# Performance work log

Measured on AMD Instinct MI355X. Metric: run time of the kernel, lower is better.

The kernel has to match this reference:

```python
import jax, jax.numpy as jnp
import numpy as np

N, L, E, H = 2, 2048, 1024, 16
DH = E // H  # head_dim = 64


def setup_inputs() -> dict:
    key = jax.random.key(0)
    ks = jax.random.split(key, 11)
    s_h = 1.0 / np.sqrt(DH)
    s_e = 1.0 / np.sqrt(E)
    return {
        "EP_q": jax.random.normal(ks[0], (N, L, E), jnp.float32),
        "EP_k": jax.random.normal(ks[1], (N, L, E), jnp.float32),
        "EP_v": jax.random.normal(ks[2], (N, L, E), jnp.float32),
        "W_q": jax.random.uniform(ks[3], (DH, DH), jnp.float32, -s_h, s_h),
        "b_q": jax.random.uniform(ks[4], (DH,), jnp.float32, -s_h, s_h),
        "W_k": jax.random.uniform(ks[5], (DH, DH), jnp.float32, -s_h, s_h),
        "b_k": jax.random.uniform(ks[6], (DH,), jnp.float32, -s_h, s_h),
        "W_v": jax.random.uniform(ks[7], (DH, DH), jnp.float32, -s_h, s_h),
        "b_v": jax.random.uniform(ks[8], (DH,), jnp.float32, -s_h, s_h),
        "W_o": jax.random.uniform(ks[9], (E, E), jnp.float32, -s_e, s_e),
        "b_o": jax.random.uniform(ks[10], (E,), jnp.float32, -s_e, s_e),
    }


def reference(EP_q, EP_k, EP_v, W_q, b_q, W_k, b_k, W_v, b_v, W_o, b_o):
    n, q_len = EP_q.shape[0], EP_q.shape[1]
    # split into heads: (N, L, H, DH)
    q = EP_q.reshape(n, q_len, H, DH)
    k = EP_k.reshape(n, EP_k.shape[1], H, DH)
    v = EP_v.reshape(n, EP_v.shape[1], H, DH)
    # per-head linear (same weights across heads), torch Linear: x @ W.T + b
    Q = q @ W_q.T + b_q
    K = k @ W_k.T + b_k
    V = v @ W_v.T + b_v
    # scores (N, H, Lq, Lk); NOTE: scaled by sqrt(embed_size) per original code
    scores = jnp.einsum("nqhd,nkhd->nhqk", Q, K) / jnp.sqrt(jnp.float32(E))
    attn = jax.nn.softmax(scores, axis=-1)
    out = jnp.einsum("nhqk,nkhd->nqhd", attn, V).reshape(n, q_len, E)
    return out @ W_o.T + b_o
```

## Files before the change

### kernel.cpp

```cpp
#include <hip/hip_runtime.h>

#define N_B 2
#define L_L 2048
#define E_E 1024
#define H_H 16
#define D_H 64
#define LDSP 72

typedef __bf16 bf16x8 __attribute__((ext_vector_type(8)));
typedef float f32x4 __attribute__((ext_vector_type(4)));
typedef short s16x8 __attribute__((ext_vector_type(8)));
typedef unsigned short u16x4 __attribute__((ext_vector_type(4)));

__device__ __forceinline__ f32x4 mfma16(bf16x8 a, bf16x8 b, f32x4 c) {
  return __builtin_amdgcn_mfma_f32_16x16x32_bf16(a, b, c, 0, 0, 0);
}

__device__ __forceinline__ unsigned short f2bf(float x) {
  unsigned int u = __float_as_uint(x);
  u = (u + 0x7fffu + ((u >> 16) & 1u)) >> 16;
  return (unsigned short)u;
}

__device__ __forceinline__ unsigned int cvtpk(float lo, float hi) {
  unsigned int r;
  asm("v_cvt_pk_bf16_f32 %0, %1, %2" : "=v"(r) : "v"(lo), "v"(hi));
  return r;
}

__device__ __forceinline__ void swap32(unsigned int& a, unsigned int& b) {
  asm("v_permlane32_swap_b32 %0, %1" : "+v"(a), "+v"(b));
}
__device__ __forceinline__ void swap16(unsigned int& a, unsigned int& b) {
  asm("v_permlane16_swap_b32 %0, %1" : "+v"(a), "+v"(b));
}

__device__ __forceinline__ float exp2a(float x) {
  float r;
  asm("v_exp_f32 %0, %1" : "=v"(r) : "v"(x));
  return r;
}

__device__ __forceinline__ void gload16(const void* g, void* l) {
  __builtin_amdgcn_global_load_lds(
      (__attribute__((address_space(1))) void*)g,
      (__attribute__((address_space(3))) void*)l, 16, 0, 0);
}

__device__ __forceinline__ bf16x8 pack_frag(const f32x4& plo, const f32x4& phi) {
  unsigned int x0 = cvtpk(plo[0], plo[1]), x1 = cvtpk(plo[2], plo[3]);
  unsigned int x2 = cvtpk(phi[0], phi[1]), x3 = cvtpk(phi[2], phi[3]);
  swap32(x0, x2); swap16(x0, x2);
  swap32(x1, x3); swap16(x1, x3);
  union { unsigned int u[4]; bf16x8 v; } f;
  f.u[0] = x0; f.u[1] = x1; f.u[2] = x2; f.u[3] = x3;
  return f.v;
}

__global__ __launch_bounds__(256) void qkv_gemm_kernel(
    const float* __restrict__ EPq, const float* __restrict__ EPk, const float* __restrict__ EPv,
    const float* __restrict__ Wq, const float* __restrict__ Wk, const float* __restrict__ Wv,
    const float* __restrict__ bq, const float* __restrict__ bk, const float* __restrict__ bv,
    const float* __restrict__ Wo, unsigned short* __restrict__ Wob,
    unsigned short* __restrict__ Qb, unsigned short* __restrict__ Kb,
    unsigned short* __restrict__ Vtb) {
  __shared__ __attribute__((aligned(16))) unsigned short Xs[64][LDSP];
  __shared__ __attribute__((aligned(16))) unsigned short Ws[64][LDSP];
  const int tid = threadIdx.x;
  const int wid = tid >> 6;
  const int lane = tid & 63;
  const int lr = lane & 15;
  const int lg = lane >> 4;
  const int nh = blockIdx.x >> 5;
  const int l0 = (blockIdx.x & 31) * 64;
  const int n = nh >> 4;
  const int h = nh & 15;
  const float SCQ = 0.03125f * 1.44269504089f;

  {
    const int i = blockIdx.x * 256 + tid;
    const float4 f = ((const float4*)Wo)[i];
    u16x4 v = { f2bf(f.x), f2bf(f.y), f2bf(f.z), f2bf(f.w) };
    *(u16x4*)&Wob[(size_t)i * 4] = v;
  }

  #pragma unroll
  for (int mat = 0; mat < 3; ++mat) {
    const float* X = (mat == 0) ? EPq : (mat == 1) ? EPk : EPv;
    const float* W = (mat == 0) ? Wq : (mat == 1) ? Wk : Wv;
    const float* bias = (mat == 0) ? bq : (mat == 1) ? bk : bv;
    const float osc = (mat == 0) ? SCQ : 1.0f;

    const float* xb = X + ((size_t)(n * L_L + l0)) * E_E + h * D_H;
    #pragma unroll
    for (int it = 0; it < 4; ++it) {
      const int idx = it * 256 + tid;
      const int row = idx >> 4, c = idx & 15;
      const float4 f = *(const float4*)(xb + (size_t)row * E_E + c * 4);
      u16x4 v = { f2bf(f.x), f2bf(f.y), f2bf(f.z), f2bf(f.w) };
      *(u16x4*)&Xs[row][c * 4] = v;
    }
    #pragma unroll
    for (int it = 0; it < 4; ++it) {
      const int idx = it * 256 + tid;
      const int row = idx >> 4, c = idx & 15;
      const float4 f = *(const float4*)(W + idx * 4);
      u16x4 v = { f2bf(f.x), f2bf(f.y), f2bf(f.z), f2bf(f.w) };
      *(u16x4*)&Ws[row][c * 4] = v;
    }
    __syncthreads();

    const bf16x8 a0 = *(const bf16x8*)&Xs[wid * 16 + lr][lg * 8];
    const bf16x8 a1 = *(const bf16x8*)&Xs[wid * 16 + lr][32 + lg * 8];
    f32x4 acc[4];
    #pragma unroll
    for (int t = 0; t < 4; ++t) {
      const float bb = bias[t * 16 + lr];
      acc[t] = f32x4{bb, bb, bb, bb};
      const bf16x8 b0 = *(const bf16x8*)&Ws[t * 16 + lr][lg * 8];
      const bf16x8 b1 = *(const bf16x8*)&Ws[t * 16 + lr][32 + lg * 8];
      acc[t] = mfma16(a0, b0, acc[t]);
      acc[t] = mfma16(a1, b1, acc[t]);
    }
    __syncthreads();

    #pragma unroll
    for (int t = 0; t < 4; ++t)
      #pragma unroll
      for (int r = 0; r < 4; ++r)
        Xs[wid * 16 + lg * 4 + r][t * 16 + lr] = f2bf(acc[t][r] * osc);
    __syncthreads();

    if (mat < 2) {
      unsigned short* dst = ((mat == 0) ? Qb : Kb) + ((size_t)nh * L_L + l0) * D_H;
      #pragma unroll
      for (int it = 0; it < 2; ++it) {
        const int idx = it * 256 + tid;
        const int row = idx >> 3, c = idx & 7;
        *(s16x8*)(dst + (size_t)row * D_H + c * 8) = *(s16x8*)&Xs[row][c * 8];
      }
    } else {
      #pragma unroll
      for (int it = 0; it < 2; ++it) {
        const int idx = it * 256 + tid;
        const int d = idx & 63, c = idx >> 6;
        s16x8 v;
        #pragma unroll
        for (int j = 0; j < 8; ++j) v[j] = (short)Xs[c * 8 + j][d];
        *(s16x8*)(Vtb + ((size_t)nh * D_H + d) * L_L + l0 + c * 8) = v;
      }
    }
    __syncthreads();
  }
}

__global__ __launch_bounds__(256, 2) void attn_mfma_kernel(
    const unsigned short* __restrict__ Qb, const unsigned short* __restrict__ Kb,
    const unsigned short* __restrict__ Vtb, unsigned short* __restrict__ Ab) {
  __shared__ __attribute__((aligned(16))) unsigned short KS[2][64][64];
  __shared__ __attribute__((aligned(16))) unsigned short VS[2][64][64];

  const int tid = threadIdx.x;
  const int wid = tid >> 6;
  const int lane = tid & 63;
  const int lr = lane & 15;
  const int lg = lane >> 4;

  const int bid = ((blockIdx.x & 7) << 6) + (blockIdx.x >> 3);
  const int nh = bid >> 4;
  const int q0w = ((bid & 15) << 7) + wid * 32;

  const unsigned short* gQ = Qb + ((size_t)nh * L_L + q0w) * D_H;
  const unsigned short* gK = Kb + (size_t)nh * L_L * D_H;
  const unsigned short* gV = Vtb + (size_t)nh * D_H * L_L;

  bf16x8 bQ[2][2];
  #pragma unroll
  for (int qb = 0; qb < 2; ++qb)
    #pragma unroll
    for (int c2 = 0; c2 < 2; ++c2)
      bQ[qb][c2] = *(const bf16x8*)(gQ + (qb * 16 + lr) * D_H + c2 * 32 + lg * 8);

  const s16x8 ones16 = {0x3F80,0x3F80,0x3F80,0x3F80,0x3F80,0x3F80,0x3F80,0x3F80};
  const bf16x8 ones = *(const bf16x8*)&ones16;

  const int srow0 = tid >> 3, sch0 = tid & 7;
  const int srow1 = srow0 + 32;
  const int kc0 = (sch0 ^ (srow0 & 7)) * 8;
  const int kc1 = (sch0 ^ (srow1 & 7)) * 8;

  #define STAGE_K(buf, ktt)                                                    \
    do {                                                                       \
      unsigned short* kd = &KS[buf][0][0];                                     \
      gload16(gK + (size_t)((ktt) * 64 + srow0) * D_H + kc0,                   \
              kd + srow0 * 64 + sch0 * 8);                                     \
      gload16(gK + (size_t)((ktt) * 64 + srow1) * D_H + kc1,                   \
              kd + srow1 * 64 + sch0 * 8);                                     \
    } while (0)
  #define STAGE_V(buf, ktt)                                                    \
    do {                                                                       \
      unsigned short* vd = &VS[buf][0][0];                                     \
      gload16(gV + (size_t)srow0 * L_L + (ktt) * 64 + kc0,                     \
              vd + srow0 * 64 + sch0 * 8);                                     \
      gload16(gV + (size_t)srow1 * L_L + (ktt) * 64 + kc1,                     \
              vd + srow1 * 64 + sch0 * 8);                                     \
    } while (0)

  f32x4 acc0[4] = {f32x4{0,0,0,0},f32x4{0,0,0,0},f32x4{0,0,0,0},f32x4{0,0,0,0}};
  f32x4 acc1[4] = {f32x4{0,0,0,0},f32x4{0,0,0,0},f32x4{0,0,0,0},f32x4{0,0,0,0}};
  f32x4 lacc0 = {0,0,0,0}, lacc1 = {0,0,0,0};
  f32x4 svA0[4], svA1[4], svB0[4], svB1[4];

  #define QKT(SQ0, SQ1, kbuf)                                                  \
    do {                                                                       \
      const char* Kc = (const char*)&KS[kbuf][0][0];                           \
      __builtin_amdgcn_s_setprio(1);                                           \
      _Pragma("unroll")                                                        \
      for (int kb = 0; kb < 4; ++kb) {                                         \
        const int row = kb * 16 + lr;                                          \
        const bf16x8 a0 = *(const bf16x8*)(Kc + row * 128 + ((lg ^ (row & 7)) << 4)); \
        const bf16x8 a1 = *(const bf16x8*)(Kc + row * 128 + (((4 + lg) ^ (row & 7)) << 4)); \
        SQ0[kb] = mfma16(a1, bQ[0][1], mfma16(a0, bQ[0][0], f32x4{0,0,0,0}));  \
        SQ1[kb] = mfma16(a1, bQ[1][1], mfma16(a0, bQ[1][0], f32x4{0,0,0,0}));  \
      }                                                                        \
      __builtin_amdgcn_s_setprio(0);                                           \
    } while (0)

  #define SMPV(SQ0, SQ1, vbuf)                                                 \
    do {                                                                       \
      _Pragma("unroll")                                                        \
      for (int kb = 0; kb < 4; ++kb)                                           \
        _Pragma("unroll")                                                      \
        for (int r = 0; r < 4; ++r) {                                          \
          SQ0[kb][r] = exp2a(SQ0[kb][r]);                                      \
          SQ1[kb][r] = exp2a(SQ1[kb][r]);                                      \
        }                                                                      \
      bf16x8 aP0[2], aP1[2];                                                   \
      aP0[0] = pack_frag(SQ0[0], SQ0[1]); aP0[1] = pack_frag(SQ0[2], SQ0[3]);  \
      aP1[0] = pack_frag(SQ1[0], SQ1[1]); aP1[1] = pack_frag(SQ1[2], SQ1[3]);  \
      const char* Vc = (const char*)&VS[vbuf][0][0];                           \
      __builtin_amdgcn_s_setprio(1);                                           \
      lacc0 = mfma16(aP0[0], ones, lacc0); lacc0 = mfma16(aP0[1], ones, lacc0);\
      lacc1 = mfma16(aP1[0], ones, lacc1); lacc1 = mfma16(aP1[1], ones, lacc1);\
      _Pragma("unroll")                                                        \
      for (int t = 0; t < 4; ++t) {                                            \
        const int row = t * 16 + lr;                                           \
        const bf16x8 v0 = *(const bf16x8*)(Vc + row * 128 + ((lg ^ (row & 7)) << 4)); \
        const bf16x8 v1 = *(const bf16x8*)(Vc + row * 128 + (((4 + lg) ^ (row & 7)) << 4)); \
        acc0[t] = mfma16(aP0[0], v0, acc0[t]); acc0[t] = mfma16(aP0[1], v1, acc0[t]); \
        acc1[t] = mfma16(aP1[0], v0, acc1[t]); acc1[t] = mfma16(aP1[1], v1, acc1[t]); \
      }                                                                        \
      __builtin_amdgcn_s_setprio(0);                                           \
    } while (0)

  STAGE_K(0, 0);
  STAGE_K(1, 1);
  STAGE_V(0, 0);
  __syncthreads();
  QKT(svA0, svA1, 0);
  __syncthreads();

  #pragma unroll 1
  for (int t2 = 0; t2 < 16; ++t2) {
    {
      const int t = 2 * t2;
      if (t2 < 15) STAGE_K(0, t + 2);
      STAGE_V(1, t + 1);
      QKT(svB0, svB1, 1);
      SMPV(svA0, svA1, 0);
      __syncthreads();
    }
    {
      const int t = 2 * t2 + 1;
      if (t2 < 15) {
        STAGE_K(1, t + 2);
        STAGE_V(0, t + 1);
        QKT(svA0, svA1, 0);
      }
      SMPV(svB0, svB1, 1);
      __syncthreads();
    }
  }
  #undef STAGE_K
  #undef STAGE_V
  #undef QKT
  #undef SMPV

  const int n = nh >> 4, h = nh & 15;
  #pragma unroll
  for (int qb = 0; qb < 2; ++qb) {
    const f32x4& la = qb ? lacc1 : lacc0;
    f32x4* ac = qb ? acc1 : acc0;
    f32x4 inv;
    #pragma unroll
    for (int r = 0; r < 4; ++r) inv[r] = 1.0f / la[r];
    const int qbase = q0w + qb * 16 + 4 * lg;
    #pragma unroll
    for (int t = 0; t < 4; ++t)
      #pragma unroll
      for (int r = 0; r < 4; ++r)
        Ab[((size_t)(n * L_L + qbase + r)) * E_E + h * D_H + t * 16 + lr] =
            f2bf(ac[t][r] * inv[r]);
  }
}

__global__ __launch_bounds__(256, 2) void out_gemm_kernel(
    const unsigned short* __restrict__ Ab, const unsigned short* __restrict__ Wob,
    const float* __restrict__ bo, float* __restrict__ out) {
  __shared__ __attribute__((aligned(16))) unsigned short As[2][64][64];
  __shared__ __attribute__((aligned(16))) unsigned short Bs[2][128][64];
  const int tid = threadIdx.x;
  const int wid = tid >> 6;
  const int lane = tid & 63;
  const int lr = lane & 15;
  const int lg = lane >> 4;

  const int bid = ((blockIdx.x & 7) << 6) + (blockIdx.x >> 3);
  const int m0 = (bid >> 3) * 64;
  const int n0 = (bid & 7) * 128;
  const int wr = wid >> 1, wc = wid & 1;

  const int r0 = tid >> 3, sc = tid & 7;
  const int scol = (sc ^ (r0 & 7)) * 8;

  #define OSTAGE(buf, kt)                                                      \
    do {                                                                       \
      unsigned short* ad = &As[buf][0][0];                                     \
      unsigned short* bd = &Bs[buf][0][0];                                     \
      gload16(Ab + (size_t)(m0 + r0) * E_E + (kt) * 64 + scol,                 \
              ad + r0 * 64 + sc * 8);                                          \
      gload16(Ab + (size_t)(m0 + r0 + 32) * E_E + (kt) * 64 + scol,            \
              ad + (r0 + 32) * 64 + sc * 8);                                   \
      gload16(Wob + (size_t)(n0 + r0) * E_E + (kt) * 64 + scol,                \
              bd + r0 * 64 + sc * 8);                                          \
      gload16(Wob + (size_t)(n0 + r0 + 32) * E_E + (kt) * 64 + scol,           \
              bd + (r0 + 32) * 64 + sc * 8);                                   \
      gload16(Wob + (size_t)(n0 + r0 + 64) * E_E + (kt) * 64 + scol,           \
              bd + (r0 + 64) * 64 + sc * 8);                                   \
      gload16(Wob + (size_t)(n0 + r0 + 96) * E_E + (kt) * 64 + scol,           \
              bd + (r0 + 96) * 64 + sc * 8);                                   \
    } while (0)

  f32x4 acc[2][4];
  #pragma unroll
  for (int mi = 0; mi < 2; ++mi)
    #pragma unroll
    for (int ni = 0; ni < 4; ++ni) {
      const float bb = bo[n0 + wc * 64 + ni * 16 + lr];
      acc[mi][ni] = f32x4{bb, bb, bb, bb};
    }

  OSTAGE(0, 0);
  __syncthreads();
  int cur = 0;

  for (int kt = 0; kt < 16; ++kt) {
    if (kt < 15) OSTAGE(cur ^ 1, kt + 1);

    const char* Ac = (const char*)&As[cur][0][0];
    const char* Bc = (const char*)&Bs[cur][0][0];
    bf16x8 af[2][2], bfr[4][2];
    #pragma unroll
    for (int mi = 0; mi < 2; ++mi) {
      const int row = wr * 32 + mi * 16 + lr;
      #pragma unroll
      for (int kb = 0; kb < 2; ++kb)
        af[mi][kb] = *(const bf16x8*)(Ac + row * 128 + (((kb * 4 + lg) ^ (row & 7)) << 4));
    }
    #pragma unroll
    for (int ni = 0; ni < 4; ++ni) {
      const int row = wc * 64 + ni * 16 + lr;
      #pragma unroll
      for (int kb = 0; kb < 2; ++kb)
        bfr[ni][kb] = *(const bf16x8*)(Bc + row * 128 + (((kb * 4 + lg) ^ (row & 7)) << 4));
    }
    __builtin_amdgcn_s_setprio(1);
    #pragma unroll
    for (int kb = 0; kb < 2; ++kb)
      #pragma unroll
      for (int mi = 0; mi < 2; ++mi)
        #pragma unroll
        for (int ni = 0; ni < 4; ++ni)
          acc[mi][ni] = mfma16(af[mi][kb], bfr[ni][kb], acc[mi][ni]);
    __builtin_amdgcn_s_setprio(0);

    __syncthreads();
    cur ^= 1;
  }
  #undef OSTAGE

  #pragma unroll
  for (int mi = 0; mi < 2; ++mi)
    #pragma unroll
    for (int ni = 0; ni < 4; ++ni) {
      const int nn = n0 + wc * 64 + ni * 16 + lr;
      #pragma unroll
      for (int r = 0; r < 4; ++r) {
        const int mm = m0 + wr * 32 + mi * 16 + lg * 4 + r;
        out[(size_t)mm * E_E + nn] = acc[mi][ni][r];
      }
    }
}

extern "C" void kernel_launch(void* const* d_in, const int* in_sizes, int n_in,
                              void* d_out, int out_size, void* d_ws, size_t ws_size,
                              hipStream_t stream) {
  const float* EPq = (const float*)d_in[0];
  const float* EPk = (const float*)d_in[1];
  const float* EPv = (const float*)d_in[2];
  const float* Wq  = (const float*)d_in[3];
  const float* bq  = (const float*)d_in[4];
  const float* Wk  = (const float*)d_in[5];
  const float* bk  = (const float*)d_in[6];
  const float* Wv  = (const float*)d_in[7];
  const float* bv  = (const float*)d_in[8];
  const float* Wo  = (const float*)d_in[9];
  const float* bo  = (const float*)d_in[10];
  float* out = (float*)d_out;

  unsigned short* ws = (unsigned short*)d_ws;
  const size_t SZ = (size_t)N_B * H_H * L_L * D_H;
  unsigned short* Qb  = ws;
  unsigned short* Kb  = Qb + SZ;
  unsigned short* Vtb = Kb + SZ;
  unsigned short* Ab  = Vtb + SZ;
  unsigned short* Wob = Ab + SZ;

  qkv_gemm_kernel<<<1024, 256, 0, stream>>>(
      EPq, EPk, EPv, Wq, Wk, Wv, bq, bk, bv, Wo, Wob, Qb, Kb, Vtb);
  attn_mfma_kernel<<<512, 256, 0, stream>>>(Qb, Kb, Vtb, Ab);
  out_gemm_kernel<<<512, 256, 0, stream>>>(Ab, Wob, bo, out);
}
```

Before: 74.21 us.

## Triple-buffer K/V tiles with explicit vmcnt waits and raw barriers in attention loop

Expands the shared K and V staging buffers from two to three and rotates read and write indices so loads for tiles two steps ahead are in flight while the current tiles are computed. The full __syncthreads is replaced by an s_waitcnt vmcnt(N) plus s_barrier, so each wave waits only for the older loads rather than draining every outstanding global-to-LDS copy. The loop is peeled with an explicit epilogue. This increases LDS use per block, which may limit occupancy, and relies on hand-counted vmcnt values being correct.

```diff
diff --git a/kernel.cpp b/kernel.cpp
--- a/kernel.cpp
+++ b/kernel.cpp
@@ -157,8 +157,8 @@
 __global__ __launch_bounds__(256, 2) void attn_mfma_kernel(
     const unsigned short* __restrict__ Qb, const unsigned short* __restrict__ Kb,
     const unsigned short* __restrict__ Vtb, unsigned short* __restrict__ Ab) {
-  __shared__ __attribute__((aligned(16))) unsigned short KS[2][64][64];
-  __shared__ __attribute__((aligned(16))) unsigned short VS[2][64][64];
+  __shared__ __attribute__((aligned(16))) unsigned short KS[3][64][64];
+  __shared__ __attribute__((aligned(16))) unsigned short VS[3][64][64];
 
   const int tid = threadIdx.x;
   const int wid = tid >> 6;
@@ -189,21 +189,19 @@
   const int kc0 = (sch0 ^ (srow0 & 7)) * 8;
   const int kc1 = (sch0 ^ (srow1 & 7)) * 8;
 
-  #define STAGE_K(buf, ktt)                                                    \
-    do {                                                                       \
-      unsigned short* kd = &KS[buf][0][0];                                     \
+  #define STAGE_K(kd, ktt)                                                     \
+    do {                                                                       \
       gload16(gK + (size_t)((ktt) * 64 + srow0) * D_H + kc0,                   \
-              kd + srow0 * 64 + sch0 * 8);                                     \
+              (kd) + srow0 * 64 + sch0 * 8);                                   \
       gload16(gK + (size_t)((ktt) * 64 + srow1) * D_H + kc1,                   \
-              kd + srow1 * 64 + sch0 * 8);                                     \
-    } while (0)
-  #define STAGE_V(buf, ktt)                                                    \
-    do {                                                                       \
-      unsigned short* vd = &VS[buf][0][0];                                     \
+              (kd) + srow1 * 64 + sch0 * 8);                                   \
+    } while (0)
+  #define STAGE_V(vd, ktt)                                                     \
+    do {                                                                       \
       gload16(gV + (size_t)srow0 * L_L + (ktt) * 64 + kc0,                     \
-              vd + srow0 * 64 + sch0 * 8);                                     \
+              (vd) + srow0 * 64 + sch0 * 8);                                   \
       gload16(gV + (size_t)srow1 * L_L + (ktt) * 64 + kc1,                     \
-              vd + srow1 * 64 + sch0 * 8);                                     \
+              (vd) + srow1 * 64 + sch0 * 8);                                   \
     } while (0)
 
   f32x4 acc0[4] = {f32x4{0,0,0,0},f32x4{0,0,0,0},f32x4{0,0,0,0},f32x4{0,0,0,0}};
@@ -211,9 +209,9 @@
   f32x4 lacc0 = {0,0,0,0}, lacc1 = {0,0,0,0};
   f32x4 svA0[4], svA1[4], svB0[4], svB1[4];
 
-  #define QKT(SQ0, SQ1, kbuf)                                                  \
-    do {                                                                       \
-      const char* Kc = (const char*)&KS[kbuf][0][0];                           \
+  #define QKT(SQ0, SQ1, Kc_)                                                   \
+    do {                                                                       \
+      const char* Kc = (const char*)(Kc_);                                     \
       __builtin_amdgcn_s_setprio(1);                                           \
       _Pragma("unroll")                                                        \
       for (int kb = 0; kb < 4; ++kb) {                                         \
@@ -226,7 +224,7 @@
       __builtin_amdgcn_s_setprio(0);                                           \
     } while (0)
 
-  #define SMPV(SQ0, SQ1, vbuf)                                                 \
+  #define SMPV(SQ0, SQ1, Vc_)                                                  \
     do {                                                                       \
       _Pragma("unroll")                                                        \
       for (int kb = 0; kb < 4; ++kb)                                           \
@@ -238,7 +236,7 @@
       bf16x8 aP0[2], aP1[2];                                                   \
       aP0[0] = pack_frag(SQ0[0], SQ0[1]); aP0[1] = pack_frag(SQ0[2], SQ0[3]);  \
       aP1[0] = pack_frag(SQ1[0], SQ1[1]); aP1[1] = pack_frag(SQ1[2], SQ1[3]);  \
-      const char* Vc = (const char*)&VS[vbuf][0][0];                           \
+      const char* Vc = (const char*)(Vc_);                                     \
       __builtin_amdgcn_s_setprio(1);                                           \
       lacc0 = mfma16(aP0[0], ones, lacc0); lacc0 = mfma16(aP0[1], ones, lacc0);\
       lacc1 = mfma16(aP1[0], ones, lacc1); lacc1 = mfma16(aP1[1], ones, lacc1);\
@@ -253,38 +251,64 @@
       __builtin_amdgcn_s_setprio(0);                                           \
     } while (0)
 
-  STAGE_K(0, 0);
-  STAGE_K(1, 1);
-  STAGE_V(0, 0);
-  __syncthreads();
-  QKT(svA0, svA1, 0);
-  __syncthreads();
-
+  #define CBAR(N)                                                              \
+    do {                                                                       \
+      asm volatile("s_waitcnt vmcnt(" #N ")" ::: "memory");                    \
+      __builtin_amdgcn_s_barrier();                                            \
+      __builtin_amdgcn_sched_barrier(0);                                       \
+    } while (0)
+
+  STAGE_K(&KS[0][0][0], 0);
+  STAGE_K(&KS[1][0][0], 1);
+  STAGE_K(&KS[2][0][0], 2);
+  STAGE_V(&VS[0][0][0], 0);
+  STAGE_V(&VS[1][0][0], 1);
+  CBAR(8);
+  QKT(svA0, svA1, &KS[0][0][0]);
+  CBAR(2);
+
+  int kr = 1, kw = 0, vw = 2, vr = 0;
   #pragma unroll 1
-  for (int t2 = 0; t2 < 16; ++t2) {
+  for (int t2 = 0; t2 < 14; ++t2) {
     {
       const int t = 2 * t2;
-      if (t2 < 15) STAGE_K(0, t + 2);
-      STAGE_V(1, t + 1);
-      QKT(svB0, svB1, 1);
-      SMPV(svA0, svA1, 0);
-      __syncthreads();
+      QKT(svB0, svB1, &KS[kr][0][0]);
+      STAGE_K(&KS[kw][0][0], t + 3);
+      STAGE_V(&VS[vw][0][0], t + 2);
+      SMPV(svA0, svA1, &VS[vr][0][0]);
+      CBAR(4);
+      kr = (kr == 2) ? 0 : kr + 1; kw = (kw == 2) ? 0 : kw + 1;
+      vw = (vw == 2) ? 0 : vw + 1; vr = (vr == 2) ? 0 : vr + 1;
     }
     {
       const int t = 2 * t2 + 1;
-      if (t2 < 15) {
-        STAGE_K(1, t + 2);
-        STAGE_V(0, t + 1);
-        QKT(svA0, svA1, 0);
-      }
-      SMPV(svB0, svB1, 1);
-      __syncthreads();
+      QKT(svA0, svA1, &KS[kr][0][0]);
+      STAGE_K(&KS[kw][0][0], t + 3);
+      STAGE_V(&VS[vw][0][0], t + 2);
+      SMPV(svB0, svB1, &VS[vr][0][0]);
+      CBAR(4);
+      kr = (kr == 2) ? 0 : kr + 1; kw = (kw == 2) ? 0 : kw + 1;
+      vw = (vw == 2) ? 0 : vw + 1; vr = (vr == 2) ? 0 : vr + 1;
     }
   }
+  QKT(svB0, svB1, &KS[2][0][0]);
+  STAGE_K(&KS[1][0][0], 31);
+  STAGE_V(&VS[0][0][0], 30);
+  SMPV(svA0, svA1, &VS[1][0][0]);
+  CBAR(4);
+  QKT(svA0, svA1, &KS[0][0][0]);
+  STAGE_V(&VS[1][0][0], 31);
+  SMPV(svB0, svB1, &VS[2][0][0]);
+  CBAR(2);
+  QKT(svB0, svB1, &KS[1][0][0]);
+  SMPV(svA0, svA1, &VS[0][0][0]);
+  CBAR(0);
+  SMPV(svB0, svB1, &VS[1][0][0]);
   #undef STAGE_K
   #undef STAGE_V
   #undef QKT
   #undef SMPV
+  #undef CBAR
 
   const int n = nh >> 4, h = nh & 15;
   #pragma unroll
```

After: 73.03 us. Within noise of the previous version (-1.6%).
